# Optimization experiments

Hardware: AMD Instinct MI355X
Metric: run time of the kernel (lower is better)

## Reference

```python
import jax, jax.numpy as jnp
import numpy as np

# dims
B, T, D, H, DFF, NTYPE = 8, 1024, 512, 8, 1024, 341
HD = D // H                    # 64 head dim
NUM_AXES = 1
DPR = D // H // (NUM_AXES + 1) # 32 dims rotated per axis
EPS = 1e-5
THETA = 10000.0


def layernorm(x, g, b):
    m = jnp.mean(x, axis=-1, keepdims=True)
    v = jnp.mean((x - m) ** 2, axis=-1, keepdims=True)
    return (x - m) * jax.lax.rsqrt(v + EPS) * g + b


def swiglu(x):
    a, gate = jnp.split(x, 2, axis=-1)
    return jax.nn.silu(gate) * a


def apply_rope(x, pos):
    # x: [B,H,T,DPR], pos: [B,T] float positions (possibly non-integer / scrambled order)
    inv_freq = 1.0 / (THETA ** (jnp.arange(0, DPR, 2, dtype=jnp.float32) / DPR))  # [DPR/2]
    freqs = pos[:, None, :, None] * inv_freq          # [B,1,T,DPR/2]
    cos = jnp.repeat(jnp.cos(freqs), 2, axis=-1)      # each freq repeated twice -> [B,1,T,DPR]
    sin = jnp.repeat(jnp.sin(freqs), 2, axis=-1)
    x1 = x[..., 0::2]
    x2 = x[..., 1::2]
    rot = jnp.stack([-x2, x1], axis=-1).reshape(x.shape)  # rotate_half, interleaved pairs
    return x * cos + rot * sin


def setup_inputs() -> dict:
    key = jax.random.key(0)
    ks = jax.random.split(key, 16)
    s = lambda d: 1.0 / np.sqrt(d)
    return {
        "x_type": jax.random.randint(ks[0], (B, T + 1), 0, NTYPE),
        "x_value": jax.random.normal(ks[1], (B, T, D), dtype=jnp.float32),
        "seq_order": jax.random.uniform(ks[2], (B, T + 1), dtype=jnp.float32) * T,
        "W_attn": jax.random.normal(ks[3], (D, 3 * D), dtype=jnp.float32) * s(D),
        "type_emb": jax.random.normal(ks[4], (NTYPE, 2 * D), dtype=jnp.float32) * 0.02,
        "ln1_g": jnp.ones((D,), jnp.float32),
        "ln1_b": jnp.zeros((D,), jnp.float32),
        "ln2_g": jnp.ones((D,), jnp.float32),
        "ln2_b": jnp.zeros((D,), jnp.float32),
        "W1": jax.random.normal(ks[5], (D, 2 * DFF), dtype=jnp.float32) * s(D),
        "b1": jnp.zeros((2 * DFF,), jnp.float32),
        "W2": jax.random.normal(ks[6], (DFF, D), dtype=jnp.float32) * s(DFF),
        "b2": jnp.zeros((D,), jnp.float32),
    }


def reference(x_type, x_value, seq_order, W_attn, type_emb, ln1_g, ln1_b, ln2_g, ln2_b, W1, b1, W2, b2):
    # --- attention sublayer ---
    h = layernorm(x_value, ln1_g, ln1_b)                  # [B,T,D]
    qkv = h @ W_attn                                      # [B,T,3D]
    q, k, v = jnp.split(qkv, 3, axis=-1)
    emb = type_emb[x_type]                                # [B,T+1,2D]
    q_embed, k_embed = jnp.split(emb, 2, axis=-1)
    q = q + q_embed[:, :-1]
    k = k + k_embed[:, 1:]
    # [B,H,T,HD]
    to_heads = lambda t: t.reshape(B, T, H, HD).transpose(0, 2, 1, 3)
    q, k, v = to_heads(q), to_heads(k), to_heads(v)
    # rotate first DPR dims with (shifted) seq_order; remaining dims untouched
    q = jnp.concatenate([apply_rope(q[..., :DPR], seq_order[:, :-1]), q[..., DPR:]], axis=-1)
    k = jnp.concatenate([apply_rope(k[..., :DPR], seq_order[:, 1:]), k[..., DPR:]], axis=-1)
    # causal SDPA
    scores = jnp.einsum("bhqd,bhkd->bhqk", q, k) / jnp.sqrt(jnp.float32(HD))
    causal = jnp.tril(jnp.ones((T, T), dtype=bool))
    scores = jnp.where(causal, scores, -jnp.inf)
    attn = jax.nn.softmax(scores, axis=-1)
    out = jnp.einsum("bhqk,bhkd->bhqd", attn, v)          # [B,H,T,HD]
    out = out.transpose(0, 2, 1, 3).reshape(B, T, D)
    x = x_value + out
    # --- SwiGLU FFN sublayer ---
    h2 = layernorm(x, ln2_g, ln2_b)
    ff = swiglu(h2 @ W1 + b1) @ W2 + b2
    return x + ff
```

## Files before the change

### kernel.cpp

```cpp
#include <hip/hip_runtime.h>
#include <stdint.h>
#include <math.h>

typedef unsigned short u16;
typedef unsigned int u32;
typedef __attribute__((ext_vector_type(8))) short bf16x8;
typedef __attribute__((ext_vector_type(4))) float f32x4;
typedef __attribute__((ext_vector_type(2))) float f32x2;
typedef __attribute__((ext_vector_type(2))) u16 u16x2;
typedef __attribute__((ext_vector_type(8))) u16 u16x8;
typedef __attribute__((ext_vector_type(2))) u32 u32x2;

#define B_ 8
#define T_ 1024
#define D_ 512
#define H_ 8
#define TP1 1025
#define QSCALE 0.1803368801111204f

__device__ __forceinline__ u16 f2b(float f) {
  union { float f; u32 u; } v; v.f = f;
  return (u16)((v.u + 0x7fffu + ((v.u >> 16) & 1u)) >> 16);
}
__device__ __forceinline__ void gld16(const void* g, void* l) {
  __builtin_amdgcn_global_load_lds((const __attribute__((address_space(1))) u32*)g,
                                   (__attribute__((address_space(3))) u32*)l, 16, 0, 0);
}
__device__ __forceinline__ f32x4 mfma16(bf16x8 a, bf16x8 b, f32x4 c) {
  return __builtin_amdgcn_mfma_f32_16x16x32_bf16(a, b, c, 0, 0, 0);
}
__device__ __forceinline__ u32 cvtpk(float lo, float hi) {
  u32 r;
  asm("v_cvt_pk_bf16_f32 %0, %1, %2" : "=v"(r) : "v"(lo), "v"(hi));
  return r;
}
union U8 { u32 u[4]; bf16x8 v; };

#define WAITV(N) asm volatile("s_waitcnt vmcnt(" #N ")" ::: "memory")

__global__ __launch_bounds__(256) void prep_kernel(const float* __restrict__ W_attn,
    const float* __restrict__ W1, const float* __restrict__ W2,
    const float* __restrict__ seq,
    u16* __restrict__ WtA, u16* __restrict__ W1i, u16* __restrict__ W2t,
    float* __restrict__ cq, float* __restrict__ sq_,
    float* __restrict__ ck, float* __restrict__ sk) {
  int bid = blockIdx.x, tid = threadIdx.x;
  if (bid >= 576) {
    int i = (bid - 576) * 256 + tid;
    int p = i & 15, bt = i >> 4, b = bt >> 10, t = bt & 1023;
    float inv = expf(-(float)p * 0.5756462732485115f);
    float aq = seq[b * TP1 + t] * inv;
    float ak = seq[b * TP1 + t + 1] * inv;
    cq[i] = cosf(aq); sq_[i] = sinf(aq);
    ck[i] = cosf(ak); sk[i] = sinf(ak);
    return;
  }
  __shared__ u16 lt[64][65];
  const float* src; u16* dst; int ld, Kd, k0, r0; bool ilv = false;
  if (bid < 192) {
    src = W_attn; dst = WtA; ld = 1536; Kd = 512;
    k0 = (bid & 7) * 64; r0 = (bid >> 3) * 64;
  } else if (bid < 448) {
    int t = bid - 192;
    src = W1; dst = W1i; ld = 2048; Kd = 512; ilv = true;
    k0 = (t & 7) * 64; r0 = (t >> 3) * 64;
  } else {
    int t = bid - 448;
    src = W2; dst = W2t; ld = 512; Kd = 1024;
    k0 = (t & 15) * 64; r0 = (t >> 4) * 64;
  }
  int nl = tid & 63;
  int scol, rloc;
  if (ilv) {
    if (nl < 32) { scol = (r0 >> 1) + nl;          rloc = ((nl >> 4) << 5) + (nl & 15); }
    else         { scol = 1024 + (r0 >> 1) + (nl - 32); rloc = (((nl - 32) >> 4) << 5) + 16 + (nl & 15); }
  } else { scol = r0 + nl; rloc = nl; }
  #pragma unroll
  for (int it = 0; it < 16; it++) {
    int kl = (tid >> 6) * 16 + it;
    lt[rloc][kl] = f2b(src[(size_t)(k0 + kl) * ld + scol]);
  }
  __syncthreads();
  #pragma unroll
  for (int it = 0; it < 16; it++) {
    int rl = (tid >> 6) * 16 + it;
    dst[(size_t)(r0 + rl) * Kd + k0 + nl] = lt[rl][nl];
  }
}

__global__ __launch_bounds__(256) void ln_kernel(const float* __restrict__ x,
    const float* __restrict__ g, const float* __restrict__ bta, u16* __restrict__ out) {
  int row = blockIdx.x * 4 + (threadIdx.x >> 6);
  int lane = threadIdx.x & 63;
  const float* xr = x + (size_t)row * D_ + lane * 8;
  f32x4 v0 = *(const f32x4*)xr;
  f32x4 v1 = *(const f32x4*)(xr + 4);
  float s = 0.f, sq = 0.f;
  #pragma unroll
  for (int j = 0; j < 4; j++) { s += v0[j] + v1[j]; sq += v0[j] * v0[j] + v1[j] * v1[j]; }
  #pragma unroll
  for (int m = 1; m < 64; m <<= 1) { s += __shfl_xor(s, m); sq += __shfl_xor(sq, m); }
  float mean = s * (1.f / D_);
  float var = sq * (1.f / D_) - mean * mean;
  float rstd = rsqrtf(var + 1e-5f);
  f32x4 g0 = *(const f32x4*)(g + lane * 8);
  f32x4 g1 = *(const f32x4*)(g + lane * 8 + 4);
  f32x4 b0 = *(const f32x4*)(bta + lane * 8);
  f32x4 b1 = *(const f32x4*)(bta + lane * 8 + 4);
  u16x8 o;
  #pragma unroll
  for (int j = 0; j < 4; j++) {
    o[j]     = f2b((v0[j] - mean) * rstd * g0[j] + b0[j]);
    o[4 + j] = f2b((v1[j] - mean) * rstd * g1[j] + b1[j]);
  }
  *(u16x8*)(out + (size_t)row * D_ + lane * 8) = o;
}


__global__ __launch_bounds__(256) void gemm_qkv(const u16* __restrict__ A,
    const u16* __restrict__ Bt,
    const int* __restrict__ x_type, const float* __restrict__ type_emb,
    const float* __restrict__ rqc, const float* __restrict__ rqs,
    const float* __restrict__ rkc, const float* __restrict__ rks,
    u16* __restrict__ qT, u16* __restrict__ kT, u16* __restrict__ vT) {
  __shared__ u16 lA[3][4096];
  __shared__ u16 lB[3][4096];
  const int K = 512, NK = 16;
  const int tid = threadIdx.x, lane = tid & 63, w = tid >> 6;
  const int wm = w >> 1, wn = w & 1;
  int swz = (blockIdx.x & 7) * 96 + (blockIdx.x >> 3);
  int byy = swz / 12, bxx = swz - byy * 12;
  const size_t bm = (size_t)byy * 128;
  const size_t bn = (size_t)bxx * 128;

  const int r0 = tid >> 2;
  const int cs = ((tid & 3) ^ ((r0 >> 1) & 3)) * 8;
  const u16* a0 = A + (bm + r0) * K + cs;
  const u16* a1 = A + (bm + 64 + r0) * K + cs;
  const u16* b0 = Bt + (bn + r0) * K + cs;
  const u16* b1p = Bt + (bn + 64 + r0) * K + cs;

  int aoff[4], boff[4];
  #pragma unroll
  for (int i = 0; i < 4; i++) {
    int ra = wm * 64 + i * 16 + (lane & 15);
    aoff[i] = ra * 64 + (((lane >> 4) ^ ((ra >> 1) & 3)) * 16);
    int rb = wn * 64 + i * 16 + (lane & 15);
    boff[i] = rb * 64 + (((lane >> 4) ^ ((rb >> 1) & 3)) * 16);
  }

  auto stage = [&](int j, int buf) {
    char* ad = (char*)lA + buf * 8192 + w * 1024;
    char* bd = (char*)lB + buf * 8192 + w * 1024;
    gld16(a0 + j * 32, ad);
    gld16(a1 + j * 32, ad + 4096);
    gld16(b0 + j * 32, bd);
    gld16(b1p + j * 32, bd + 4096);
  };
  f32x4 acc[4][4] = {};
  auto compute = [&](int buf) {
    const char* lAc = (const char*)lA + buf * 8192;
    const char* lBc = (const char*)lB + buf * 8192;
    bf16x8 af[4], bf[4];
    #pragma unroll
    for (int i = 0; i < 4; i++) af[i] = *(const bf16x8*)(lAc + aoff[i]);
    #pragma unroll
    for (int n = 0; n < 4; n++) bf[n] = *(const bf16x8*)(lBc + boff[n]);
    __builtin_amdgcn_s_setprio(1);
    #pragma unroll
    for (int i = 0; i < 4; i++)
      #pragma unroll
      for (int n = 0; n < 4; n++)
        acc[i][n] = mfma16(af[i], bf[n], acc[i][n]);
    __builtin_amdgcn_s_setprio(0);
  };

  stage(0, 0);
  stage(1, 1);
  int cur = 0;
  for (int j = 0; j < NK - 1; j++) {
    WAITV(4);
    __builtin_amdgcn_s_barrier();
    if (j + 2 < NK) { int nb = cur + 2; if (nb >= 3) nb -= 3; stage(j + 2, nb); }
    compute(cur);
    cur = (cur + 1 == 3) ? 0 : cur + 1;
  }
  WAITV(0);
  __builtin_amdgcn_s_barrier();
  compute(cur);

  const int region = (int)(bn >> 9);
  #pragma unroll
  for (int i = 0; i < 4; i++) {
    #pragma unroll
    for (int jj = 0; jj < 4; jj++) {
      int row = (int)bm + wm * 64 + i * 16 + (lane >> 4) * 4 + jj;
      int b = row >> 10, t = row & 1023;
      if (region == 0) {
        int ty = x_type[b * TP1 + t];
        #pragma unroll
        for (int n = 0; n < 4; n++) {
          int cloc = (int)bn + wn * 64 + n * 16 + (lane & 15);
          int h = cloc >> 6, hd = cloc & 63;
          float v = acc[i][n][jj] + type_emb[(size_t)ty * 1024 + cloc];
          float vp = __shfl_xor(v, 1);
          if (hd < 32) {
            int p = hd >> 1;
            float c = rqc[row * 16 + p], s = rqs[row * 16 + p];
            v = (hd & 1) ? (v * c + vp * s) : (v * c - vp * s);
          }
          qT[((size_t)(b * 8 + h) * T_ + t) * 64 + hd] = f2b(v * QSCALE);
        }
      } else if (region == 1) {
        int ty = x_type[b * TP1 + t + 1];
        #pragma unroll
        for (int n = 0; n < 4; n++) {
          int cloc = (int)bn - 512 + wn * 64 + n * 16 + (lane & 15);
          int h = cloc >> 6, hd = cloc & 63;
          float v = acc[i][n][jj] + type_emb[(size_t)ty * 1024 + 512 + cloc];
          float vp = __shfl_xor(v, 1);
          if (hd < 32) {
            int p = hd >> 1;
            float c = rkc[row * 16 + p], s = rks[row * 16 + p];
            v = (hd & 1) ? (v * c + vp * s) : (v * c - vp * s);
          }
          kT[((size_t)(b * 8 + h) * T_ + t) * 64 + hd] = f2b(v);
        }
      } else {
        #pragma unroll
        for (int n = 0; n < 4; n++) {
          int cloc = (int)bn - 1024 + wn * 64 + n * 16 + (lane & 15);
          int h = cloc >> 6, hd = cloc & 63;
          vT[((size_t)(b * 8 + h) * 64 + hd) * T_ + t] = f2b(acc[i][n][jj]);
        }
      }
    }
  }
}

__global__ __launch_bounds__(256) void gemm_ff1(const u16* __restrict__ A,
    const u16* __restrict__ Bt, const float* __restrict__ b1,
    u16* __restrict__ outp) {
  __shared__ u16 lA[3][4096];
  __shared__ u16 lB[3][4096];
  const int K = 512, NK = 16;
  const int tid = threadIdx.x, lane = tid & 63, w = tid >> 6;
  const int wm = w >> 1, wn = w & 1;
  int swz = (blockIdx.x & 7) * 128 + (blockIdx.x >> 3);
  int byy = swz >> 4, bxx = swz & 15;
  const size_t bm = (size_t)byy * 128;
  const size_t bn = (size_t)bxx * 128;

  const int r0 = tid >> 2;
  const int cs = ((tid & 3) ^ ((r0 >> 1) & 3)) * 8;
  const u16* a0 = A + (bm + r0) * K + cs;
  const u16* a1 = A + (bm + 64 + r0) * K + cs;
  const u16* b0 = Bt + (bn + r0) * K + cs;
  const u16* b1p = Bt + (bn + 64 + r0) * K + cs;

  int aoff[4], boff[4];
  #pragma unroll
  for (int i = 0; i < 4; i++) {
    int ra = wm * 64 + i * 16 + (lane & 15);
    aoff[i] = ra * 64 + (((lane >> 4) ^ ((ra >> 1) & 3)) * 16);
    int rb = wn * 64 + i * 16 + (lane & 15);
    boff[i] = rb * 64 + (((lane >> 4) ^ ((rb >> 1) & 3)) * 16);
  }

  auto stage = [&](int j, int buf) {
    char* ad = (char*)lA + buf * 8192 + w * 1024;
    char* bd = (char*)lB + buf * 8192 + w * 1024;
    gld16(a0 + j * 32, ad);
    gld16(a1 + j * 32, ad + 4096);
    gld16(b0 + j * 32, bd);
    gld16(b1p + j * 32, bd + 4096);
  };
  f32x4 acc[4][4] = {};
  auto compute = [&](int buf) {
    const char* lAc = (const char*)lA + buf * 8192;
    const char* lBc = (const char*)lB + buf * 8192;
    bf16x8 af[4], bf[4];
    #pragma unroll
    for (int i = 0; i < 4; i++) af[i] = *(const bf16x8*)(lAc + aoff[i]);
    #pragma unroll
    for (int n = 0; n < 4; n++) bf[n] = *(const bf16x8*)(lBc + boff[n]);
    __builtin_amdgcn_s_setprio(1);
    #pragma unroll
    for (int i = 0; i < 4; i++)
      #pragma unroll
      for (int n = 0; n < 4; n++)
        acc[i][n] = mfma16(af[i], bf[n], acc[i][n]);
    __builtin_amdgcn_s_setprio(0);
  };

  stage(0, 0);
  stage(1, 1);
  int cur = 0;
  for (int j = 0; j < NK - 1; j++) {
    WAITV(4);
    __builtin_amdgcn_s_barrier();
    if (j + 2 < NK) { int nb = cur + 2; if (nb >= 3) nb -= 3; stage(j + 2, nb); }
    compute(cur);
    cur = (cur + 1 == 3) ? 0 : cur + 1;
  }
  WAITV(0);
  __builtin_amdgcn_s_barrier();
  compute(cur);

  #pragma unroll
  for (int np = 0; np < 2; np++) {
    int c = ((int)bn >> 1) + wn * 32 + np * 16 + (lane & 15);
    float bav = b1[c], bgv = b1[1024 + c];
    #pragma unroll
    for (int i = 0; i < 4; i++) {
      #pragma unroll
      for (int jj = 0; jj < 4; jj++) {
        int row = (int)bm + wm * 64 + i * 16 + (lane >> 4) * 4 + jj;
        float av = acc[i][2 * np][jj] + bav;
        float gv = acc[i][2 * np + 1][jj] + bgv;
        float sg = gv / (1.f + expf(-gv));
        outp[(size_t)row * 1024 + c] = f2b(sg * av);
      }
    }
  }
}

__global__ __launch_bounds__(512) void gemm_ff2(const u16* __restrict__ A,
    const u16* __restrict__ Bt, const float* __restrict__ bias,
    float* __restrict__ C) {
  __shared__ u16 lA[3][4096];
  __shared__ u16 lB[3][4096];
  const int K = 1024, N = 512, NK = 32;
  const int tid = threadIdx.x, lane = tid & 63, w = tid >> 6;
  const int wm = w >> 2, wn = w & 3;
  int swz = (blockIdx.x & 7) * 32 + (blockIdx.x >> 3);
  int byy = swz >> 2, bxx = swz & 3;
  const size_t bm = (size_t)byy * 128;
  const size_t bn = (size_t)bxx * 128;

  const int r0 = tid >> 2;
  const int cs = ((tid & 3) ^ ((r0 >> 1) & 3)) * 8;
  const u16* a0 = A + (bm + r0) * K + cs;
  const u16* b0 = Bt + (bn + r0) * K + cs;

  int aoff[4], boff[2];
  #pragma unroll
  for (int i = 0; i < 4; i++) {
    int ra = wm * 64 + i * 16 + (lane & 15);
    aoff[i] = ra * 64 + (((lane >> 4) ^ ((ra >> 1) & 3)) * 16);
  }
  #pragma unroll
  for (int n = 0; n < 2; n++) {
    int rb = wn * 32 + n * 16 + (lane & 15);
    boff[n] = rb * 64 + (((lane >> 4) ^ ((rb >> 1) & 3)) * 16);
  }

  auto stage = [&](int j, int buf) {
    gld16(a0 + j * 32, (char*)lA + buf * 8192 + w * 1024);
    gld16(b0 + j * 32, (char*)lB + buf * 8192 + w * 1024);
  };
  f32x4 acc[4][2] = {};
  auto compute = [&](int buf) {
    const char* lAc = (const char*)lA + buf * 8192;
    const char* lBc = (const char*)lB + buf * 8192;
    bf16x8 af[4], bf[2];
    #pragma unroll
    for (int i = 0; i < 4; i++) af[i] = *(const bf16x8*)(lAc + aoff[i]);
    #pragma unroll
    for (int n = 0; n < 2; n++) bf[n] = *(const bf16x8*)(lBc + boff[n]);
    __builtin_amdgcn_s_setprio(1);
    #pragma unroll
    for (int i = 0; i < 4; i++)
      #pragma unroll
      for (int n = 0; n < 2; n++)
        acc[i][n] = mfma16(af[i], bf[n], acc[i][n]);
    __builtin_amdgcn_s_setprio(0);
  };

  stage(0, 0);
  stage(1, 1);
  int cur = 0;
  for (int j = 0; j < NK - 1; j++) {
    WAITV(2);
    __builtin_amdgcn_s_barrier();
    if (j + 2 < NK) { int nb = cur + 2; if (nb >= 3) nb -= 3; stage(j + 2, nb); }
    compute(cur);
    cur = (cur + 1 == 3) ? 0 : cur + 1;
  }
  WAITV(0);
  __builtin_amdgcn_s_barrier();
  compute(cur);

  #pragma unroll
  for (int i = 0; i < 4; i++) {
    size_t mrow = bm + wm * 64 + i * 16 + (lane >> 4) * 4;
    #pragma unroll
    for (int n = 0; n < 2; n++) {
      size_t col = bn + wn * 32 + n * 16 + (lane & 15);
      float bv = bias[col];
      #pragma unroll
      for (int jj = 0; jj < 4; jj++) {
        size_t idx = (mrow + jj) * (size_t)N + col;
        C[idx] = acc[i][n][jj] + bv + C[idx];
      }
    }
  }
}

__global__ __launch_bounds__(512) void attn_kernel(const u16* __restrict__ qT,
    const u16* __restrict__ kT, const u16* __restrict__ vT,
    const float* __restrict__ xv, float* __restrict__ X) {
  int s0 = (blockIdx.x & 7) * 64 + (blockIdx.x >> 3);
  const int bh = s0 >> 3;
  const int qp = 7 - (s0 & 7);
  const int b = bh >> 3, h = bh & 7;
  const int tid = threadIdx.x, lane = tid & 63, w = tid >> 6;
  const int q = lane & 15, g = lane >> 4;
  __shared__ u16 lK[3][4096];
  __shared__ u16 lV[3][4096];

  const int qrow0 = qp * 128 + w * 16;
  bf16x8 qf[2];
  {
    const u16* qp_ = qT + ((size_t)bh * T_ + qrow0 + q) * 64 + g * 8;
    qf[0] = *(const bf16x8*)qp_;
    qf[1] = *(const bf16x8*)(qp_ + 32);
  }
  f32x4 acc[4] = {};
  float mr = -1e30f, lr = 0.f;

  const int sr = tid >> 3;
  const int scs = ((tid & 7) ^ (sr & 7)) * 8;
  const u16* kb = kT + ((size_t)bh * T_ + sr) * 64 + scs;
  const u16* vb = vT + ((size_t)bh * 64 + sr) * T_ + scs;

  auto stage = [&](int j, int buf) {
    gld16(kb + (size_t)j * 4096, (char*)lK + buf * 8192 + w * 1024);
    gld16(vb + j * 64, (char*)lV + buf * 8192 + w * 1024);
  };
  auto compute = [&](int j, int buf) {
    const char* lKc = (const char*)lK + buf * 8192;
    const char* lVc = (const char*)lV + buf * 8192;
    if (j * 64 > qrow0 + 15) return;
    f32x4 s[4] = {};
    __builtin_amdgcn_s_setprio(1);
    #pragma unroll
    for (int ka = 0; ka < 2; ka++) {
      #pragma unroll
      for (int n = 0; n < 4; n++) {
        bf16x8 kf = *(const bf16x8*)(lKc + (n * 16 + q) * 128 +
                                     (((ka * 4 + g) ^ (q & 7)) * 16));
        s[n] = mfma16(kf, qf[ka], s[n]);
      }
    }
    __builtin_amdgcn_s_setprio(0);
    if (j * 64 + 63 > qrow0) {
      int qrow = qrow0 + q;
      #pragma unroll
      for (int n = 0; n < 4; n++)
        #pragma unroll
        for (int i = 0; i < 4; i++)
          if (j * 64 + n * 16 + g * 4 + i > qrow) s[n][i] = -1e30f;
    }
    float mt = fmaxf(fmaxf(fmaxf(s[0][0], s[0][1]), fmaxf(s[0][2], s[0][3])),
                     fmaxf(fmaxf(s[1][0], s[1][1]), fmaxf(s[1][2], s[1][3])));
    mt = fmaxf(mt, fmaxf(fmaxf(fmaxf(s[2][0], s[2][1]), fmaxf(s[2][2], s[2][3])),
                         fmaxf(fmaxf(s[3][0], s[3][1]), fmaxf(s[3][2], s[3][3]))));
    mt = fmaxf(mt, __shfl_xor(mt, 16));
    mt = fmaxf(mt, __shfl_xor(mt, 32));
    if (__any(mt > mr + 8.f)) {
      float mnew = fmaxf(mr, mt);
      float sc = exp2f(mr - mnew);
      mr = mnew;
      lr *= sc;
      #pragma unroll
      for (int t = 0; t < 4; t++) acc[t] *= sc;
    }
    float p[4][4];
    float ps = 0.f;
    #pragma unroll
    for (int n = 0; n < 4; n++)
      #pragma unroll
      for (int i = 0; i < 4; i++) { p[n][i] = exp2f(s[n][i] - mr); ps += p[n][i]; }
    ps += __shfl_xor(ps, 16);
    ps += __shfl_xor(ps, 32);
    lr += ps;
    U8 pa[2];
    #pragma unroll
    for (int kt = 0; kt < 2; kt++) {
      pa[kt].u[0] = cvtpk(p[2 * kt][0], p[2 * kt][1]);
      pa[kt].u[1] = cvtpk(p[2 * kt][2], p[2 * kt][3]);
      pa[kt].u[2] = cvtpk(p[2 * kt + 1][0], p[2 * kt + 1][1]);
      pa[kt].u[3] = cvtpk(p[2 * kt + 1][2], p[2 * kt + 1][3]);
    }
    __builtin_amdgcn_s_setprio(1);
    #pragma unroll
    for (int t = 0; t < 4; t++) {
      const char* vr = lVc + (t * 16 + q) * 128 + (g & 1) * 8;
      #pragma unroll
      for (int kt = 0; kt < 2; kt++) {
        u32x2 lo = *(const u32x2*)(vr + (((kt * 4 + (g >> 1)) ^ (q & 7)) * 16));
        u32x2 hi = *(const u32x2*)(vr + (((kt * 4 + 2 + (g >> 1)) ^ (q & 7)) * 16));
        U8 af;
        af.u[0] = lo[0]; af.u[1] = lo[1]; af.u[2] = hi[0]; af.u[3] = hi[1];
        acc[t] = mfma16(af.v, pa[kt].v, acc[t]);
      }
    }
    __builtin_amdgcn_s_setprio(0);
  };

  const int jmax = 2 * qp + 2;
  stage(0, 0);
  stage(1, 1);
  int cur = 0;
  for (int j = 0; j < jmax - 1; j++) {
    WAITV(2);
    __builtin_amdgcn_s_barrier();
    if (j + 2 < jmax) { int nb = cur + 2; if (nb >= 3) nb -= 3; stage(j + 2, nb); }
    compute(j, cur);
    cur = (cur + 1 == 3) ? 0 : cur + 1;
  }
  WAITV(0);
  __builtin_amdgcn_s_barrier();
  compute(jmax - 1, cur);

  {
    float inv = 1.f / lr;
    size_t base = ((size_t)b * T_ + qrow0 + q) * D_ + h * 64 + g * 4;
    #pragma unroll
    for (int t = 0; t < 4; t++) {
      f32x4 r = *(const f32x4*)(xv + base + t * 16);
      f32x4 o;
      #pragma unroll
      for (int i = 0; i < 4; i++) o[i] = r[i] + acc[t][i] * inv;
      *(f32x4*)(X + base + t * 16) = o;
    }
  }
}

extern "C" void kernel_launch(void* const* d_in, const int* in_sizes, int n_in,
                              void* d_out, int out_size, void* d_ws, size_t ws_size,
                              hipStream_t stream) {
  const int*   x_type   = (const int*)d_in[0];
  const float* x_value  = (const float*)d_in[1];
  const float* seq      = (const float*)d_in[2];
  const float* W_attn   = (const float*)d_in[3];
  const float* type_emb = (const float*)d_in[4];
  const float* ln1_g    = (const float*)d_in[5];
  const float* ln1_b    = (const float*)d_in[6];
  const float* ln2_g    = (const float*)d_in[7];
  const float* ln2_b    = (const float*)d_in[8];
  const float* W1       = (const float*)d_in[9];
  const float* b1       = (const float*)d_in[10];
  const float* W2       = (const float*)d_in[11];
  const float* b2       = (const float*)d_in[12];
  float* out = (float*)d_out;
  char* ws = (char*)d_ws;

  u16*   WtA  = (u16*)(ws + 0);
  u16*   W1i  = (u16*)(ws + 1572864);
  u16*   W2t  = (u16*)(ws + 3670016);
  float* rqc  = (float*)(ws + 4718592);
  float* rqs  = (float*)(ws + 5242880);
  float* rkc  = (float*)(ws + 5767168);
  float* rks  = (float*)(ws + 6291456);
  u16*   hbuf = (u16*)(ws + 6815744);
  u16*   qTb  = (u16*)(ws + 15204352);
  u16*   kTb  = (u16*)(ws + 23592960);
  u16*   vTb  = (u16*)(ws + 31981568);
  u16*   ff1a = (u16*)(ws + 15204352);

  prep_kernel<<<1088, 256, 0, stream>>>(W_attn, W1, W2, seq, WtA, W1i, W2t,
                                        rqc, rqs, rkc, rks);
  ln_kernel<<<B_ * T_ / 4, 256, 0, stream>>>(x_value, ln1_g, ln1_b, hbuf);
  gemm_qkv<<<768, 256, 0, stream>>>(hbuf, WtA, x_type, type_emb,
                                    rqc, rqs, rkc, rks, qTb, kTb, vTb);
  attn_kernel<<<512, 512, 0, stream>>>(qTb, kTb, vTb, x_value, out);
  ln_kernel<<<B_ * T_ / 4, 256, 0, stream>>>(out, ln2_g, ln2_b, hbuf);
  gemm_ff1<<<1024, 256, 0, stream>>>(hbuf, W1i, b1, ff1a);
  gemm_ff2<<<256, 512, 0, stream>>>(ff1a, W2t, b2, out);
}
```

Baseline: 143.3 us.

## Enlarge FF1 tiles to 256x256 and make attention per-wave without LDS

The FF1 GEMM moves from 128x128 tiles with a 3-stage LDS pipeline to 256x256 tiles with 512 threads, double buffering and __syncthreads, which raises operand reuse but simplifies the prefetch pipeline and uses more registers. The attention kernel is rewritten so each wave independently handles a 16-row query strip. It loads K and V fragments straight from global memory into registers, with K prefetched one step ahead, and drops the shared-memory staging and barriers. This removes synchronisation and gives finer causal load balance, at the cost of redundant global/L2 reads of K/V across waves and less latency hiding.

After: 201.8 us. 40.8% more time.

```diff
diff --git a/kernel.cpp b/kernel.cpp
--- a/kernel.cpp
+++ b/kernel.cpp
@@ -115,7 +115,6 @@
   }
   *(u16x8*)(out + (size_t)row * D_ + lane * 8) = o;
 }
-
 
 __global__ __launch_bounds__(256) void gemm_qkv(const u16* __restrict__ A,
     const u16* __restrict__ Bt,
@@ -238,84 +237,79 @@
   }
 }
 
-__global__ __launch_bounds__(256) void gemm_ff1(const u16* __restrict__ A,
+__global__ __launch_bounds__(512) void gemm_ff1(const u16* __restrict__ A,
     const u16* __restrict__ Bt, const float* __restrict__ b1,
     u16* __restrict__ outp) {
-  __shared__ u16 lA[3][4096];
-  __shared__ u16 lB[3][4096];
-  const int K = 512, NK = 16;
+  __shared__ u16 lA[2][8192];
+  __shared__ u16 lB[2][8192];
+  const int K = 512;
   const int tid = threadIdx.x, lane = tid & 63, w = tid >> 6;
-  const int wm = w >> 1, wn = w & 1;
-  int swz = (blockIdx.x & 7) * 128 + (blockIdx.x >> 3);
-  int byy = swz >> 4, bxx = swz & 15;
-  const size_t bm = (size_t)byy * 128;
-  const size_t bn = (size_t)bxx * 128;
+  const int wm = w >> 2, wn = w & 3;
+  int swz = (blockIdx.x & 7) * 32 + (blockIdx.x >> 3);
+  int byy = swz >> 3, bxx = swz & 7;
+  const size_t bm = (size_t)byy * 256;
+  const size_t bn = (size_t)bxx * 256;
 
   const int r0 = tid >> 2;
   const int cs = ((tid & 3) ^ ((r0 >> 1) & 3)) * 8;
   const u16* a0 = A + (bm + r0) * K + cs;
-  const u16* a1 = A + (bm + 64 + r0) * K + cs;
+  const u16* a1 = A + (bm + 128 + r0) * K + cs;
   const u16* b0 = Bt + (bn + r0) * K + cs;
-  const u16* b1p = Bt + (bn + 64 + r0) * K + cs;
-
-  int aoff[4], boff[4];
-  #pragma unroll
-  for (int i = 0; i < 4; i++) {
-    int ra = wm * 64 + i * 16 + (lane & 15);
+  const u16* b1p = Bt + (bn + 128 + r0) * K + cs;
+
+  int aoff[8], boff[4];
+  #pragma unroll
+  for (int i = 0; i < 8; i++) {
+    int ra = wm * 128 + i * 16 + (lane & 15);
     aoff[i] = ra * 64 + (((lane >> 4) ^ ((ra >> 1) & 3)) * 16);
-    int rb = wn * 64 + i * 16 + (lane & 15);
-    boff[i] = rb * 64 + (((lane >> 4) ^ ((rb >> 1) & 3)) * 16);
-  }
-
-  auto stage = [&](int j, int buf) {
-    char* ad = (char*)lA + buf * 8192 + w * 1024;
-    char* bd = (char*)lB + buf * 8192 + w * 1024;
-    gld16(a0 + j * 32, ad);
-    gld16(a1 + j * 32, ad + 4096);
-    gld16(b0 + j * 32, bd);
-    gld16(b1p + j * 32, bd + 4096);
+  }
+  #pragma unroll
+  for (int n = 0; n < 4; n++) {
+    int rb = wn * 64 + n * 16 + (lane & 15);
+    boff[n] = rb * 64 + (((lane >> 4) ^ ((rb >> 1) & 3)) * 16);
+  }
+
+  auto stage = [&](int k0, int buf) {
+    char* ad = (char*)lA + buf * 16384 + w * 1024;
+    char* bd = (char*)lB + buf * 16384 + w * 1024;
+    gld16(a0 + k0, ad);
+    gld16(a1 + k0, ad + 8192);
+    gld16(b0 + k0, bd);
+    gld16(b1p + k0, bd + 8192);
   };
-  f32x4 acc[4][4] = {};
-  auto compute = [&](int buf) {
-    const char* lAc = (const char*)lA + buf * 8192;
-    const char* lBc = (const char*)lB + buf * 8192;
-    bf16x8 af[4], bf[4];
-    #pragma unroll
-    for (int i = 0; i < 4; i++) af[i] = *(const bf16x8*)(lAc + aoff[i]);
+
+  f32x4 acc[8][4] = {};
+  stage(0, 0);
+  __syncthreads();
+  int cur = 0;
+  for (int k0 = 0; k0 < K; k0 += 32) {
+    if (k0 + 32 < K) stage(k0 + 32, cur ^ 1);
+    const char* lAc = (const char*)lA + cur * 16384;
+    const char* lBc = (const char*)lB + cur * 16384;
+    bf16x8 bf[4];
     #pragma unroll
     for (int n = 0; n < 4; n++) bf[n] = *(const bf16x8*)(lBc + boff[n]);
     __builtin_amdgcn_s_setprio(1);
     #pragma unroll
-    for (int i = 0; i < 4; i++)
+    for (int i = 0; i < 8; i++) {
+      bf16x8 af = *(const bf16x8*)(lAc + aoff[i]);
       #pragma unroll
       for (int n = 0; n < 4; n++)
-        acc[i][n] = mfma16(af[i], bf[n], acc[i][n]);
+        acc[i][n] = mfma16(af, bf[n], acc[i][n]);
+    }
     __builtin_amdgcn_s_setprio(0);
-  };
-
-  stage(0, 0);
-  stage(1, 1);
-  int cur = 0;
-  for (int j = 0; j < NK - 1; j++) {
-    WAITV(4);
-    __builtin_amdgcn_s_barrier();
-    if (j + 2 < NK) { int nb = cur + 2; if (nb >= 3) nb -= 3; stage(j + 2, nb); }
-    compute(cur);
-    cur = (cur + 1 == 3) ? 0 : cur + 1;
-  }
-  WAITV(0);
-  __builtin_amdgcn_s_barrier();
-  compute(cur);
-
+    __syncthreads();
+    cur ^= 1;
+  }
   #pragma unroll
   for (int np = 0; np < 2; np++) {
     int c = ((int)bn >> 1) + wn * 32 + np * 16 + (lane & 15);
     float bav = b1[c], bgv = b1[1024 + c];
     #pragma unroll
-    for (int i = 0; i < 4; i++) {
+    for (int i = 0; i < 8; i++) {
       #pragma unroll
       for (int jj = 0; jj < 4; jj++) {
-        int row = (int)bm + wm * 64 + i * 16 + (lane >> 4) * 4 + jj;
+        int row = (int)bm + wm * 128 + i * 16 + (lane >> 4) * 4 + jj;
         float av = acc[i][2 * np][jj] + bav;
         float gv = acc[i][2 * np + 1][jj] + bgv;
         float sg = gv / (1.f + expf(-gv));
@@ -407,54 +401,66 @@
   }
 }
 
-__global__ __launch_bounds__(512) void attn_kernel(const u16* __restrict__ qT,
+__global__ __launch_bounds__(256) void attn_kernel(const u16* __restrict__ qT,
     const u16* __restrict__ kT, const u16* __restrict__ vT,
     const float* __restrict__ xv, float* __restrict__ X) {
-  int s0 = (blockIdx.x & 7) * 64 + (blockIdx.x >> 3);
-  const int bh = s0 >> 3;
-  const int qp = 7 - (s0 & 7);
+  const int w = threadIdx.x >> 6, lane = threadIdx.x & 63;
+  const int f = ((int)blockIdx.x >> 3) * 4 + w;
+  const int xcd = blockIdx.x & 7;
+  const int bh = xcd * 8 + (f & 7);
+  const int sp = 63 - (f >> 3);
   const int b = bh >> 3, h = bh & 7;
-  const int tid = threadIdx.x, lane = tid & 63, w = tid >> 6;
   const int q = lane & 15, g = lane >> 4;
-  __shared__ u16 lK[3][4096];
-  __shared__ u16 lV[3][4096];
-
-  const int qrow0 = qp * 128 + w * 16;
+  const int qrow0 = sp * 16;
+  const int jmax = (sp >> 2) + 1;
+
   bf16x8 qf[2];
   {
     const u16* qp_ = qT + ((size_t)bh * T_ + qrow0 + q) * 64 + g * 8;
     qf[0] = *(const bf16x8*)qp_;
     qf[1] = *(const bf16x8*)(qp_ + 32);
   }
+  const u16* kl = kT + (size_t)bh * 65536 + q * 64 + g * 8;
+  const u16* vl = vT + (size_t)bh * 65536 + (size_t)q * 1024 + g * 4;
+
   f32x4 acc[4] = {};
   float mr = -1e30f, lr = 0.f;
 
-  const int sr = tid >> 3;
-  const int scs = ((tid & 7) ^ (sr & 7)) * 8;
-  const u16* kb = kT + ((size_t)bh * T_ + sr) * 64 + scs;
-  const u16* vb = vT + ((size_t)bh * 64 + sr) * T_ + scs;
-
-  auto stage = [&](int j, int buf) {
-    gld16(kb + (size_t)j * 4096, (char*)lK + buf * 8192 + w * 1024);
-    gld16(vb + j * 64, (char*)lV + buf * 8192 + w * 1024);
-  };
-  auto compute = [&](int j, int buf) {
-    const char* lKc = (const char*)lK + buf * 8192;
-    const char* lVc = (const char*)lV + buf * 8192;
-    if (j * 64 > qrow0 + 15) return;
+  bf16x8 kc[8];
+  #pragma unroll
+  for (int n = 0; n < 4; n++)
+    #pragma unroll
+    for (int ka = 0; ka < 2; ka++)
+      kc[n * 2 + ka] = *(const bf16x8*)(kl + n * 1024 + ka * 32);
+
+  for (int j = 0; j < jmax; j++) {
+    u32x2 vlo[8], vhi[8];
+    #pragma unroll
+    for (int t = 0; t < 4; t++) {
+      const u16* vp = vl + (size_t)t * 16384 + j * 64;
+      #pragma unroll
+      for (int kt = 0; kt < 2; kt++) {
+        vlo[t * 2 + kt] = *(const u32x2*)(vp + kt * 32);
+        vhi[t * 2 + kt] = *(const u32x2*)(vp + kt * 32 + 16);
+      }
+    }
     f32x4 s[4] = {};
     __builtin_amdgcn_s_setprio(1);
     #pragma unroll
-    for (int ka = 0; ka < 2; ka++) {
-      #pragma unroll
-      for (int n = 0; n < 4; n++) {
-        bf16x8 kf = *(const bf16x8*)(lKc + (n * 16 + q) * 128 +
-                                     (((ka * 4 + g) ^ (q & 7)) * 16));
-        s[n] = mfma16(kf, qf[ka], s[n]);
-      }
-    }
+    for (int ka = 0; ka < 2; ka++)
+      #pragma unroll
+      for (int n = 0; n < 4; n++)
+        s[n] = mfma16(kc[n * 2 + ka], qf[ka], s[n]);
     __builtin_amdgcn_s_setprio(0);
-    if (j * 64 + 63 > qrow0) {
+    if (j + 1 < jmax) {
+      const u16* kn = kl + (size_t)(j + 1) * 4096;
+      #pragma unroll
+      for (int n = 0; n < 4; n++)
+        #pragma unroll
+        for (int ka = 0; ka < 2; ka++)
+          kc[n * 2 + ka] = *(const bf16x8*)(kn + n * 1024 + ka * 32);
+    }
+    if (j == jmax - 1) {
       int qrow = qrow0 + q;
       #pragma unroll
       for (int n = 0; n < 4; n++)
@@ -496,34 +502,16 @@
     __builtin_amdgcn_s_setprio(1);
     #pragma unroll
     for (int t = 0; t < 4; t++) {
-      const char* vr = lVc + (t * 16 + q) * 128 + (g & 1) * 8;
       #pragma unroll
       for (int kt = 0; kt < 2; kt++) {
-        u32x2 lo = *(const u32x2*)(vr + (((kt * 4 + (g >> 1)) ^ (q & 7)) * 16));
-        u32x2 hi = *(const u32x2*)(vr + (((kt * 4 + 2 + (g >> 1)) ^ (q & 7)) * 16));
         U8 af;
-        af.u[0] = lo[0]; af.u[1] = lo[1]; af.u[2] = hi[0]; af.u[3] = hi[1];
+        af.u[0] = vlo[t * 2 + kt][0]; af.u[1] = vlo[t * 2 + kt][1];
+        af.u[2] = vhi[t * 2 + kt][0]; af.u[3] = vhi[t * 2 + kt][1];
         acc[t] = mfma16(af.v, pa[kt].v, acc[t]);
       }
     }
     __builtin_amdgcn_s_setprio(0);
-  };
-
-  const int jmax = 2 * qp + 2;
-  stage(0, 0);
-  stage(1, 1);
-  int cur = 0;
-  for (int j = 0; j < jmax - 1; j++) {
-    WAITV(2);
-    __builtin_amdgcn_s_barrier();
-    if (j + 2 < jmax) { int nb = cur + 2; if (nb >= 3) nb -= 3; stage(j + 2, nb); }
-    compute(j, cur);
-    cur = (cur + 1 == 3) ? 0 : cur + 1;
-  }
-  WAITV(0);
-  __builtin_amdgcn_s_barrier();
-  compute(jmax - 1, cur);
-
+  }
   {
     float inv = 1.f / lr;
     size_t base = ((size_t)b * T_ + qrow0 + q) * D_ + h * 64 + g * 4;
@@ -575,8 +563,8 @@
   ln_kernel<<<B_ * T_ / 4, 256, 0, stream>>>(x_value, ln1_g, ln1_b, hbuf);
   gemm_qkv<<<768, 256, 0, stream>>>(hbuf, WtA, x_type, type_emb,
                                     rqc, rqs, rkc, rks, qTb, kTb, vTb);
-  attn_kernel<<<512, 512, 0, stream>>>(qTb, kTb, vTb, x_value, out);
+  attn_kernel<<<1024, 256, 0, stream>>>(qTb, kTb, vTb, x_value, out);
   ln_kernel<<<B_ * T_ / 4, 256, 0, stream>>>(out, ln2_g, ln2_b, hbuf);
-  gemm_ff1<<<1024, 256, 0, stream>>>(hbuf, W1i, b1, ff1a);
+  gemm_ff1<<<256, 512, 0, stream>>>(hbuf, W1i, b1, ff1a);
   gemm_ff2<<<256, 512, 0, stream>>>(ff1a, W2t, b2, out);
 }
```
